# Performance work log

Hardware: AMD Instinct MI355X
Metric: run time of the kernel (lower is better)

Reference implementation:

```python
import jax, jax.numpy as jnp
import numpy as np

NE = 200000   # num_entities
NR = 16       # num_relations
D  = 128      # embed_dim
B  = 4096     # batch
S  = 64       # neighbors per node
L  = 2        # num_layers
H  = 4        # attention heads (hardcoded in module)


def _ln(x, g, b, eps=1e-5):
    m = jnp.mean(x, -1, keepdims=True)
    v = jnp.mean((x - m) ** 2, -1, keepdims=True)
    return (x - m) * jax.lax.rsqrt(v + eps) * g + b


def setup_inputs() -> dict:
    key = jax.random.key(0)
    ks = jax.random.split(key, 12)
    s = 0.05
    return {
        'drug_entity_indices': jax.random.randint(ks[0], (B,), 0, NE),
        'adj_entity': jax.random.randint(ks[1], (B, S), 0, NE),
        'adj_relation': jax.random.randint(ks[2], (B, S), 0, NR),
        'edge_weights': jax.random.uniform(ks[3], (B, S), dtype=jnp.float32),
        'entity_emb': jax.random.normal(ks[4], (NE, D), jnp.float32) * s,
        'W_rgcn': jax.random.normal(ks[5], (L, NR, D, D), jnp.float32) * s,
        'res_w': jax.random.normal(ks[6], (L, D, D), jnp.float32) * s,
        'res_b': jnp.zeros((L, D), jnp.float32),
        'proj_w': jax.random.normal(ks[7], (L, D, D), jnp.float32) * s,
        'proj_b': jnp.zeros((L, D), jnp.float32),
        'ln_g': jnp.ones((L, D), jnp.float32),
        'ln_b': jnp.zeros((L, D), jnp.float32),
        'in_proj_w': jax.random.normal(ks[8], (3 * D, D), jnp.float32) * s,
        'in_proj_b': jnp.zeros((3 * D,), jnp.float32),
        'out_proj_w': jax.random.normal(ks[9], (D, D), jnp.float32) * s,
        'out_proj_b': jnp.zeros((D,), jnp.float32),
        'fln_g': jnp.ones((D,), jnp.float32),
        'fln_b': jnp.zeros((D,), jnp.float32),
    }


def reference(drug_entity_indices, adj_entity, adj_relation, edge_weights,
              entity_emb, W_rgcn, res_w, res_b, proj_w, proj_b, ln_g, ln_b,
              in_proj_w, in_proj_b, out_proj_w, out_proj_b, fln_g, fln_b):
    node = entity_emb[drug_entity_indices]           # [B,D] combined_emb
    nbr = entity_emb[adj_entity]                     # [B,S,D]
    # Route each edge to its relation: sum_s nbr*ew*[rel==r] then one GEMM per relation
    # (mathematically identical to the per-relation masked matmul loop in torch).
    onehot = jax.nn.one_hot(adj_relation, NR, dtype=node.dtype)      # [B,S,R]
    pre = jnp.einsum('bsd,bsr->brd', nbr * edge_weights[..., None], onehot)
    outs = []
    for l in range(L):
        msgs = jnp.einsum('brd,rde->be', pre, W_rgcn[l])             # [B,D]
        h = jax.nn.relu(node + msgs + node @ res_w[l].T + res_b[l])  # RGCNAggregator
        node = _ln(h @ proj_w[l].T + proj_b[l] + node, ln_g[l], ln_b[l])
        outs.append(node)
    x = jnp.stack(outs, 0)                           # [L,B,D] seq-first
    qkv = x @ in_proj_w.T + in_proj_b
    q, k, v = jnp.split(qkv, 3, axis=-1)
    hd = D // H
    def heads(t):
        return t.reshape(L, B, H, hd).transpose(1, 2, 0, 3)          # [B,H,L,hd]
    q, k, v = heads(q), heads(k), heads(v)
    att = jax.nn.softmax(jnp.einsum('bhld,bhmd->bhlm', q, k) / np.sqrt(hd).astype(np.float32), axis=-1)
    o = jnp.einsum('bhlm,bhmd->bhld', att, v).transpose(2, 0, 1, 3).reshape(L, B, D)
    o = o @ out_proj_w.T + out_proj_b
    return _ln(o.mean(0), fln_g, fln_b)              # [B,D]
```

## Files before the change

### kernel.cpp

```cpp
#include <hip/hip_runtime.h>
#include <math.h>

#define NRREL 16
#define DDIM 128
#define BBATCH 4096
#define SNBR 64

typedef __attribute__((ext_vector_type(8))) short short8;
typedef __attribute__((ext_vector_type(4))) float floatx4;

__device__ __forceinline__ unsigned short f2bf(float f) {
    unsigned u = __builtin_bit_cast(unsigned, f);
    u += 0x7fffu + ((u >> 16) & 1u);
    return (unsigned short)(u >> 16);
}
__device__ __forceinline__ float bf2f(unsigned short u) {
    return __builtin_bit_cast(float, ((unsigned)u) << 16);
}

extern "C" __global__ __launch_bounds__(256)
void k_wconv(const float* __restrict__ W_rgcn, const float* __restrict__ res_w,
             const float* __restrict__ proj_w, const float* __restrict__ in_w,
             const float* __restrict__ out_w,
             unsigned short* __restrict__ Wcat, unsigned short* __restrict__ resw,
             unsigned short* __restrict__ projw, unsigned short* __restrict__ inw,
             unsigned short* __restrict__ outw)
{
    const int bid = blockIdx.x, t = threadIdx.x;
    if (bid < 64) {
        __shared__ float tileT[128 * 65];
        const int l = bid >> 5, k0 = (bid & 31) * 64;
        #pragma unroll
        for (int i = 0; i < 8; ++i) {
            int flat = t + 256 * i;
            int k = flat >> 5, c = flat & 31;
            float4 v = *(const float4*)(W_rgcn + ((size_t)(l * 2048 + k0 + k)) * 128 + 4 * c);
            tileT[(4 * c + 0) * 65 + k] = v.x;
            tileT[(4 * c + 1) * 65 + k] = v.y;
            tileT[(4 * c + 2) * 65 + k] = v.z;
            tileT[(4 * c + 3) * 65 + k] = v.w;
        }
        __syncthreads();
        const int e = t >> 1, half = t & 1;
        #pragma unroll
        for (int m = 0; m < 4; ++m) {
            int kk = 32 * half + 8 * m;
            short8 o;
            #pragma unroll
            for (int j = 0; j < 8; ++j) o[j] = (short)f2bf(tileT[e * 65 + kk + j]);
            *(short8*)(Wcat + ((size_t)(l * 128 + e)) * 2048 + k0 + kk) = o;
        }
    } else {
        int j4 = (bid - 64) * 1024 + t * 4;
        const float* src; unsigned short* dst; int off;
        if (j4 < 32768)       { src = res_w;  dst = resw;  off = j4; }
        else if (j4 < 65536)  { src = proj_w; dst = projw; off = j4 - 32768; }
        else if (j4 < 114688) { src = in_w;   dst = inw;   off = j4 - 65536; }
        else                  { src = out_w;  dst = outw;  off = j4 - 114688; }
        float4 v = *(const float4*)(src + off);
        ushort4 o = { f2bf(v.x), f2bf(v.y), f2bf(v.z), f2bf(v.w) };
        *(ushort4*)(dst + off) = o;
    }
}

extern "C" __global__ __launch_bounds__(256)
void k_gather(const int* __restrict__ drug, const int* __restrict__ adj_e,
              const int* __restrict__ adj_r, const float* __restrict__ ew,
              const float* __restrict__ emb,
              unsigned short* __restrict__ pre_bf, float* __restrict__ node_f)
{
    __shared__ float rows[64 * 132];
    __shared__ int   srel[64];
    __shared__ float swt[64];
    __shared__ int   sent[64];
    const int b = blockIdx.x, t = threadIdx.x;
    if (t < 64) {
        sent[t] = adj_e[b * SNBR + t];
        srel[t] = adj_r[b * SNBR + t];
        swt[t]  = ew[b * SNBR + t];
    }
    __syncthreads();
    #pragma unroll
    for (int i = 0; i < 8; ++i) {
        int flat = t + 256 * i;
        int s = flat >> 5, c = flat & 31;
        float w = swt[s];
        float4 v = *(const float4*)(emb + (size_t)sent[s] * DDIM + 4 * c);
        float4 sv; sv.x = v.x * w; sv.y = v.y * w; sv.z = v.z * w; sv.w = v.w * w;
        *(float4*)(rows + s * 132 + 4 * c) = sv;
    }
    if (t < 32) {
        float4 nf = *(const float4*)(emb + (size_t)drug[b] * DDIM + 4 * t);
        *(float4*)(node_f + (size_t)b * DDIM + 4 * t) = nf;
    }
    __syncthreads();
    const int r = t >> 4, g = t & 15;
    float acc[8] = {0.f, 0.f, 0.f, 0.f, 0.f, 0.f, 0.f, 0.f};
    #pragma unroll 4
    for (int s = 0; s < SNBR; ++s) {
        if (srel[s] == r) {
            const float* p = rows + s * 132 + 8 * g;
            #pragma unroll
            for (int j = 0; j < 8; ++j) acc[j] += p[j];
        }
    }
    short8 o;
    #pragma unroll
    for (int j = 0; j < 8; ++j) o[j] = (short)f2bf(acc[j]);
    *(short8*)(pre_bf + (size_t)b * 2048 + r * DDIM + 8 * g) = o;
}

extern "C" __global__ __launch_bounds__(256)
void k_msgs(const unsigned short* __restrict__ pre_bf,
            const unsigned short* __restrict__ Wcat, float* __restrict__ part)
{
    const int wave = threadIdx.x >> 6, wm = wave >> 1, wn = wave & 1;
    const int r0 = blockIdx.x * 64 + wm * 32;
    const int c0 = blockIdx.y * 64 + wn * 32;
    const int koff = blockIdx.z * 512;
    const int lane = threadIdx.x & 63, l15 = lane & 15, q = lane >> 4;
    floatx4 acc[2][2] = {};
    const unsigned short* a0 = pre_bf + (size_t)(r0 + l15) * 2048 + koff + q * 8;
    const unsigned short* a1 = a0 + (size_t)16 * 2048;
    const unsigned short* b0 = Wcat + (size_t)(c0 + l15) * 2048 + koff + q * 8;
    const unsigned short* b1 = b0 + (size_t)16 * 2048;
    #pragma unroll 2
    for (int k = 0; k < 512; k += 32) {
        short8 A0 = *(const short8*)(a0 + k);
        short8 A1 = *(const short8*)(a1 + k);
        short8 B0 = *(const short8*)(b0 + k);
        short8 B1 = *(const short8*)(b1 + k);
        acc[0][0] = __builtin_amdgcn_mfma_f32_16x16x32_bf16(A0, B0, acc[0][0], 0, 0, 0);
        acc[0][1] = __builtin_amdgcn_mfma_f32_16x16x32_bf16(A0, B1, acc[0][1], 0, 0, 0);
        acc[1][0] = __builtin_amdgcn_mfma_f32_16x16x32_bf16(A1, B0, acc[1][0], 0, 0, 0);
        acc[1][1] = __builtin_amdgcn_mfma_f32_16x16x32_bf16(A1, B1, acc[1][1], 0, 0, 0);
    }
    float* dst = part + (size_t)blockIdx.z * BBATCH * 256;
    for (int mi = 0; mi < 2; ++mi)
        for (int ni = 0; ni < 2; ++ni) {
            int gc = c0 + ni * 16 + l15;
            #pragma unroll
            for (int r = 0; r < 4; ++r) {
                int gr = r0 + mi * 16 + 4 * q + r;
                dst[(size_t)gr * 256 + gc] = acc[mi][ni][r];
            }
        }
}

extern "C" __global__ __launch_bounds__(256)
void k_tail(const float* __restrict__ node_fg, const float* __restrict__ part,
            const unsigned short* __restrict__ resw, const unsigned short* __restrict__ projw,
            const float* __restrict__ res_b, const float* __restrict__ proj_b,
            const float* __restrict__ ln_g, const float* __restrict__ ln_b,
            const unsigned short* __restrict__ inw, const float* __restrict__ in_b,
            const unsigned short* __restrict__ outw, const float* __restrict__ out_b,
            const float* __restrict__ fg, const float* __restrict__ fb,
            float* __restrict__ outp)
{
    __shared__ float          node_ln[32 * 132];
    __shared__ unsigned short node_b16[32 * 136];
    __shared__ unsigned short h_b16[32 * 136];
    __shared__ float          msum[32 * 260];
    __shared__ unsigned short xs_l[64 * 136];
    __shared__ unsigned short qkvl[64 * 392];
    __shared__ float          psum[2][32], psq[2][32];

    const int t = threadIdx.x, w = t >> 6, lane = t & 63, l15 = lane & 15, q = lane >> 4;
    const int r0 = blockIdx.x * 32;
    const int wm = w & 1, wn = w >> 1;

    #pragma unroll
    for (int i = 0; i < 4; ++i) {
        int flat = t + 256 * i;
        int rr = flat >> 5, c = flat & 31;
        float4 v = *(const float4*)(node_fg + (size_t)(r0 + rr) * DDIM + 4 * c);
        *(float4*)(node_ln + rr * 132 + 4 * c) = v;
        ushort4 o = { f2bf(v.x), f2bf(v.y), f2bf(v.z), f2bf(v.w) };
        *(ushort4*)(node_b16 + rr * 136 + 4 * c) = o;
    }
    #pragma unroll
    for (int i = 0; i < 8; ++i) {
        int flat = t + 256 * i;
        int rr = flat >> 6, c = flat & 63;
        float4 s = {0.f, 0.f, 0.f, 0.f};
        #pragma unroll
        for (int kc = 0; kc < 4; ++kc) {
            float4 v = *(const float4*)(part + ((size_t)kc * BBATCH + r0 + rr) * 256 + 4 * c);
            s.x += v.x; s.y += v.y; s.z += v.z; s.w += v.w;
        }
        *(float4*)(msum + rr * 260 + 4 * c) = s;
    }
    __syncthreads();

    for (int l = 0; l < 2; ++l) {
        {
            const unsigned short* Bw = resw + (size_t)l * DDIM * DDIM;
            floatx4 acc[4] = {};
            const unsigned short* ap = node_b16 + (16 * wm + l15) * 136 + 8 * q;
            #pragma unroll
            for (int kk = 0; kk < DDIM; kk += 32) {
                short8 A = *(const short8*)(ap + kk);
                #pragma unroll
                for (int ni = 0; ni < 4; ++ni) {
                    short8 B = *(const short8*)(Bw + (size_t)(64 * wn + ni * 16 + l15) * DDIM + kk + 8 * q);
                    acc[ni] = __builtin_amdgcn_mfma_f32_16x16x32_bf16(A, B, acc[ni], 0, 0, 0);
                }
            }
            #pragma unroll
            for (int ni = 0; ni < 4; ++ni) {
                int gc = 64 * wn + ni * 16 + l15;
                float rb = res_b[l * DDIM + gc];
                #pragma unroll
                for (int r = 0; r < 4; ++r) {
                    int lr = 16 * wm + 4 * q + r;
                    float v = acc[ni][r] + rb + node_ln[lr * 132 + gc] + msum[lr * 260 + l * DDIM + gc];
                    h_b16[lr * 136 + gc] = f2bf(v > 0.f ? v : 0.f);
                }
            }
        }
        __syncthreads();
        {
            const unsigned short* Bw = projw + (size_t)l * DDIM * DDIM;
            floatx4 acc[4] = {};
            const unsigned short* ap = h_b16 + (16 * wm + l15) * 136 + 8 * q;
            #pragma unroll
            for (int kk = 0; kk < DDIM; kk += 32) {
                short8 A = *(const short8*)(ap + kk);
                #pragma unroll
                for (int ni = 0; ni < 4; ++ni) {
                    short8 B = *(const short8*)(Bw + (size_t)(64 * wn + ni * 16 + l15) * DDIM + kk + 8 * q);
                    acc[ni] = __builtin_amdgcn_mfma_f32_16x16x32_bf16(A, B, acc[ni], 0, 0, 0);
                }
            }
            float vv[4][4];
            float s4[4] = {0, 0, 0, 0}, sq4[4] = {0, 0, 0, 0};
            #pragma unroll
            for (int ni = 0; ni < 4; ++ni) {
                int gc = 64 * wn + ni * 16 + l15;
                float pb = proj_b[l * DDIM + gc];
                #pragma unroll
                for (int r = 0; r < 4; ++r) {
                    int lr = 16 * wm + 4 * q + r;
                    float v = acc[ni][r] + pb + node_ln[lr * 132 + gc];
                    vv[ni][r] = v; s4[r] += v; sq4[r] += v * v;
                }
            }
            #pragma unroll
            for (int r = 0; r < 4; ++r)
                #pragma unroll
                for (int off = 8; off >= 1; off >>= 1) {
                    s4[r] += __shfl_xor(s4[r], off, 64);
                    sq4[r] += __shfl_xor(sq4[r], off, 64);
                }
            if (l15 == 0) {
                #pragma unroll
                for (int r = 0; r < 4; ++r) {
                    psum[wn][16 * wm + 4 * q + r] = s4[r];
                    psq[wn][16 * wm + 4 * q + r] = sq4[r];
                }
            }
            __syncthreads();
            #pragma unroll
            for (int ni = 0; ni < 4; ++ni) {
                int gc = 64 * wn + ni * 16 + l15;
                float g = ln_g[l * DDIM + gc], bb = ln_b[l * DDIM + gc];
                #pragma unroll
                for (int r = 0; r < 4; ++r) {
                    int lr = 16 * wm + 4 * q + r;
                    float mean = (psum[0][lr] + psum[1][lr]) * (1.f / DDIM);
                    float var = (psq[0][lr] + psq[1][lr]) * (1.f / DDIM) - mean * mean;
                    float val = (vv[ni][r] - mean) * rsqrtf(var + 1e-5f) * g + bb;
                    node_ln[lr * 132 + gc] = val;
                    unsigned short ub = f2bf(val);
                    node_b16[lr * 136 + gc] = ub;
                    xs_l[(2 * lr + l) * 136 + gc] = ub;
                }
            }
            __syncthreads();
        }
    }

    {
        floatx4 acc[24] = {};
        const unsigned short* ap = xs_l + (16 * w + l15) * 136 + 8 * q;
        #pragma unroll
        for (int kk = 0; kk < DDIM; kk += 32) {
            short8 A = *(const short8*)(ap + kk);
            #pragma unroll
            for (int ni = 0; ni < 24; ++ni) {
                short8 B = *(const short8*)(inw + (size_t)(ni * 16 + l15) * DDIM + kk + 8 * q);
                acc[ni] = __builtin_amdgcn_mfma_f32_16x16x32_bf16(A, B, acc[ni], 0, 0, 0);
            }
        }
        #pragma unroll
        for (int ni = 0; ni < 24; ++ni) {
            int gc = ni * 16 + l15;
            float ib = in_b[gc];
            #pragma unroll
            for (int r = 0; r < 4; ++r)
                qkvl[(16 * w + 4 * q + r) * 392 + gc] = f2bf(acc[ni][r] + ib);
        }
    }
    __syncthreads();

    {
        int g = t >> 3, j = t & 7;
        const unsigned short* row0 = qkvl + (2 * g) * 392;
        const unsigned short* row1 = qkvl + (2 * g + 1) * 392;
        float p00 = 0.f, p01 = 0.f, p10 = 0.f, p11 = 0.f;
        #pragma unroll
        for (int dd = 0; dd < 16; ++dd) {
            int d = 16 * j + dd;
            float q0 = bf2f(row0[d]), k0 = bf2f(row0[128 + d]);
            float q1 = bf2f(row1[d]), k1 = bf2f(row1[128 + d]);
            p00 = fmaf(q0, k0, p00); p01 = fmaf(q0, k1, p01);
            p10 = fmaf(q1, k0, p10); p11 = fmaf(q1, k1, p11);
        }
        p00 += __shfl_xor(p00, 1, 64); p01 += __shfl_xor(p01, 1, 64);
        p10 += __shfl_xor(p10, 1, 64); p11 += __shfl_xor(p11, 1, 64);
        const float sc = 0.17677669529663687f;
        p00 *= sc; p01 *= sc; p10 *= sc; p11 *= sc;
        float m0 = fmaxf(p00, p01), e00 = expf(p00 - m0), e01 = expf(p01 - m0);
        float i0 = 1.f / (e00 + e01);
        float m1 = fmaxf(p10, p11), e10 = expf(p10 - m1), e11 = expf(p11 - m1);
        float i1 = 1.f / (e10 + e11);
        #pragma unroll
        for (int dd = 0; dd < 16; ++dd) {
            int d = 16 * j + dd;
            float v0 = bf2f(row0[256 + d]), v1 = bf2f(row1[256 + d]);
            xs_l[(2 * g) * 136 + d]     = f2bf((e00 * v0 + e01 * v1) * i0);
            xs_l[(2 * g + 1) * 136 + d] = f2bf((e10 * v0 + e11 * v1) * i1);
        }
    }
    __syncthreads();

    {
        floatx4 acc[8] = {};
        const unsigned short* ap = xs_l + (16 * w + l15) * 136 + 8 * q;
        #pragma unroll
        for (int kk = 0; kk < DDIM; kk += 32) {
            short8 A = *(const short8*)(ap + kk);
            #pragma unroll
            for (int ni = 0; ni < 8; ++ni) {
                short8 B = *(const short8*)(outw + (size_t)(ni * 16 + l15) * DDIM + kk + 8 * q);
                acc[ni] = __builtin_amdgcn_mfma_f32_16x16x32_bf16(A, B, acc[ni], 0, 0, 0);
            }
        }
        float av[2][8];
        float s[2] = {0, 0}, sq[2] = {0, 0};
        #pragma unroll
        for (int ni = 0; ni < 8; ++ni) {
            int gc = ni * 16 + l15;
            float ob = out_b[gc];
            #pragma unroll
            for (int rr = 0; rr < 2; ++rr) {
                float v = 0.5f * (acc[ni][2 * rr] + acc[ni][2 * rr + 1]) + ob;
                av[rr][ni] = v; s[rr] += v; sq[rr] += v * v;
            }
        }
        #pragma unroll
        for (int rr = 0; rr < 2; ++rr)
            #pragma unroll
            for (int off = 8; off >= 1; off >>= 1) {
                s[rr] += __shfl_xor(s[rr], off, 64);
                sq[rr] += __shfl_xor(sq[rr], off, 64);
            }
        #pragma unroll
        for (int ni = 0; ni < 8; ++ni) {
            int gc = ni * 16 + l15;
            float g = fg[gc], bb = fb[gc];
            #pragma unroll
            for (int rr = 0; rr < 2; ++rr) {
                int bg = r0 + 8 * w + 2 * q + rr;
                float mean = s[rr] * (1.f / DDIM);
                float var = sq[rr] * (1.f / DDIM) - mean * mean;
                outp[(size_t)bg * DDIM + gc] = (av[rr][ni] - mean) * rsqrtf(var + 1e-5f) * g + bb;
            }
        }
    }
}

extern "C" void kernel_launch(void* const* d_in, const int* in_sizes, int n_in,
                              void* d_out, int out_size, void* d_ws, size_t ws_size,
                              hipStream_t stream) {
    const int*   drug_idx = (const int*)d_in[0];
    const int*   adj_ent  = (const int*)d_in[1];
    const int*   adj_rel  = (const int*)d_in[2];
    const float* ew       = (const float*)d_in[3];
    const float* emb      = (const float*)d_in[4];
    const float* W_rgcn   = (const float*)d_in[5];
    const float* res_w    = (const float*)d_in[6];
    const float* res_b    = (const float*)d_in[7];
    const float* proj_w   = (const float*)d_in[8];
    const float* proj_b   = (const float*)d_in[9];
    const float* ln_g     = (const float*)d_in[10];
    const float* ln_b     = (const float*)d_in[11];
    const float* in_w     = (const float*)d_in[12];
    const float* in_b     = (const float*)d_in[13];
    const float* out_w    = (const float*)d_in[14];
    const float* out_b    = (const float*)d_in[15];
    const float* fg       = (const float*)d_in[16];
    const float* fb       = (const float*)d_in[17];
    float* outp = (float*)d_out;

    char* ws = (char*)d_ws;
    size_t off = 0;
    auto alloc = [&](size_t bytes) { size_t o = off; off = (off + bytes + 255) & ~(size_t)255; return o; };
    unsigned short* pre_bf  = (unsigned short*)(ws + alloc((size_t)BBATCH * 2048 * 2));
    float*          node_f  = (float*)         (ws + alloc((size_t)BBATCH * 128 * 4));
    float*          part    = (float*)         (ws + alloc((size_t)4 * BBATCH * 256 * 4));
    unsigned short* Wcat    = (unsigned short*)(ws + alloc((size_t)256 * 2048 * 2));
    unsigned short* resw    = (unsigned short*)(ws + alloc((size_t)2 * 128 * 128 * 2));
    unsigned short* projw   = (unsigned short*)(ws + alloc((size_t)2 * 128 * 128 * 2));
    unsigned short* inw     = (unsigned short*)(ws + alloc((size_t)384 * 128 * 2));
    unsigned short* outw    = (unsigned short*)(ws + alloc((size_t)128 * 128 * 2));

    hipLaunchKernelGGL(k_wconv, dim3(192), dim3(256), 0, stream,
                       W_rgcn, res_w, proj_w, in_w, out_w, Wcat, resw, projw, inw, outw);
    hipLaunchKernelGGL(k_gather, dim3(BBATCH), dim3(256), 0, stream,
                       drug_idx, adj_ent, adj_rel, ew, emb, pre_bf, node_f);
    hipLaunchKernelGGL(k_msgs, dim3(64, 4, 4), dim3(256), 0, stream, pre_bf, Wcat, part);
    hipLaunchKernelGGL(k_tail, dim3(128), dim3(256), 0, stream,
                       node_f, part, resw, projw, res_b, proj_b, ln_g, ln_b,
                       inw, in_b, outw, out_b, fg, fb, outp);
}
```

Measured before the change: 267.3 us.

## Fuse all stages into one cooperative kernel with grid-wide syncs

Merges the weight conversion, gather, message GEMM and tail kernels into a single persistent cooperative kernel of 1024 blocks, separating the stages with grid syncs. If the cooperative launch fails it falls back to three ordinary launches. The tail now handles 8 rows per block instead of 32, which spreads it over more blocks but reloads the weights more often. The aim is to remove the launch gaps between kernels and the tail's low parallelism, at the cost of grid-barrier overhead and an occupancy cap of 4 blocks per CU with shared memory held in a union.

```diff
diff --git a/kernel.cpp b/kernel.cpp
--- a/kernel.cpp
+++ b/kernel.cpp
@@ -1,5 +1,8 @@
 #include <hip/hip_runtime.h>
+#include <hip/hip_cooperative_groups.h>
 #include <math.h>
+
+namespace cg = cooperative_groups;
 
 #define NRREL 16
 #define DDIM 128
@@ -18,363 +21,369 @@
     return __builtin_bit_cast(float, ((unsigned)u) << 16);
 }
 
-extern "C" __global__ __launch_bounds__(256)
-void k_wconv(const float* __restrict__ W_rgcn, const float* __restrict__ res_w,
-             const float* __restrict__ proj_w, const float* __restrict__ in_w,
-             const float* __restrict__ out_w,
-             unsigned short* __restrict__ Wcat, unsigned short* __restrict__ resw,
-             unsigned short* __restrict__ projw, unsigned short* __restrict__ inw,
-             unsigned short* __restrict__ outw)
-{
-    const int bid = blockIdx.x, t = threadIdx.x;
-    if (bid < 64) {
-        __shared__ float tileT[128 * 65];
-        const int l = bid >> 5, k0 = (bid & 31) * 64;
-        #pragma unroll
-        for (int i = 0; i < 8; ++i) {
-            int flat = t + 256 * i;
-            int k = flat >> 5, c = flat & 31;
-            float4 v = *(const float4*)(W_rgcn + ((size_t)(l * 2048 + k0 + k)) * 128 + 4 * c);
-            tileT[(4 * c + 0) * 65 + k] = v.x;
-            tileT[(4 * c + 1) * 65 + k] = v.y;
-            tileT[(4 * c + 2) * 65 + k] = v.z;
-            tileT[(4 * c + 3) * 65 + k] = v.w;
-        }
-        __syncthreads();
-        const int e = t >> 1, half = t & 1;
-        #pragma unroll
-        for (int m = 0; m < 4; ++m) {
-            int kk = 32 * half + 8 * m;
-            short8 o;
-            #pragma unroll
-            for (int j = 0; j < 8; ++j) o[j] = (short)f2bf(tileT[e * 65 + kk + j]);
-            *(short8*)(Wcat + ((size_t)(l * 128 + e)) * 2048 + k0 + kk) = o;
-        }
-    } else {
-        int j4 = (bid - 64) * 1024 + t * 4;
-        const float* src; unsigned short* dst; int off;
-        if (j4 < 32768)       { src = res_w;  dst = resw;  off = j4; }
-        else if (j4 < 65536)  { src = proj_w; dst = projw; off = j4 - 32768; }
-        else if (j4 < 114688) { src = in_w;   dst = inw;   off = j4 - 65536; }
-        else                  { src = out_w;  dst = outw;  off = j4 - 114688; }
-        float4 v = *(const float4*)(src + off);
-        ushort4 o = { f2bf(v.x), f2bf(v.y), f2bf(v.z), f2bf(v.w) };
-        *(ushort4*)(dst + off) = o;
-    }
-}
-
-extern "C" __global__ __launch_bounds__(256)
-void k_gather(const int* __restrict__ drug, const int* __restrict__ adj_e,
-              const int* __restrict__ adj_r, const float* __restrict__ ew,
-              const float* __restrict__ emb,
-              unsigned short* __restrict__ pre_bf, float* __restrict__ node_f)
-{
-    __shared__ float rows[64 * 132];
-    __shared__ int   srel[64];
-    __shared__ float swt[64];
-    __shared__ int   sent[64];
-    const int b = blockIdx.x, t = threadIdx.x;
-    if (t < 64) {
-        sent[t] = adj_e[b * SNBR + t];
-        srel[t] = adj_r[b * SNBR + t];
-        swt[t]  = ew[b * SNBR + t];
-    }
-    __syncthreads();
-    #pragma unroll
-    for (int i = 0; i < 8; ++i) {
-        int flat = t + 256 * i;
-        int s = flat >> 5, c = flat & 31;
-        float w = swt[s];
-        float4 v = *(const float4*)(emb + (size_t)sent[s] * DDIM + 4 * c);
-        float4 sv; sv.x = v.x * w; sv.y = v.y * w; sv.z = v.z * w; sv.w = v.w * w;
-        *(float4*)(rows + s * 132 + 4 * c) = sv;
-    }
-    if (t < 32) {
-        float4 nf = *(const float4*)(emb + (size_t)drug[b] * DDIM + 4 * t);
-        *(float4*)(node_f + (size_t)b * DDIM + 4 * t) = nf;
-    }
-    __syncthreads();
-    const int r = t >> 4, g = t & 15;
-    float acc[8] = {0.f, 0.f, 0.f, 0.f, 0.f, 0.f, 0.f, 0.f};
-    #pragma unroll 4
-    for (int s = 0; s < SNBR; ++s) {
-        if (srel[s] == r) {
-            const float* p = rows + s * 132 + 8 * g;
-            #pragma unroll
-            for (int j = 0; j < 8; ++j) acc[j] += p[j];
-        }
-    }
-    short8 o;
-    #pragma unroll
-    for (int j = 0; j < 8; ++j) o[j] = (short)f2bf(acc[j]);
-    *(short8*)(pre_bf + (size_t)b * 2048 + r * DDIM + 8 * g) = o;
-}
-
-extern "C" __global__ __launch_bounds__(256)
-void k_msgs(const unsigned short* __restrict__ pre_bf,
-            const unsigned short* __restrict__ Wcat, float* __restrict__ part)
-{
-    const int wave = threadIdx.x >> 6, wm = wave >> 1, wn = wave & 1;
-    const int r0 = blockIdx.x * 64 + wm * 32;
-    const int c0 = blockIdx.y * 64 + wn * 32;
-    const int koff = blockIdx.z * 512;
-    const int lane = threadIdx.x & 63, l15 = lane & 15, q = lane >> 4;
-    floatx4 acc[2][2] = {};
-    const unsigned short* a0 = pre_bf + (size_t)(r0 + l15) * 2048 + koff + q * 8;
-    const unsigned short* a1 = a0 + (size_t)16 * 2048;
-    const unsigned short* b0 = Wcat + (size_t)(c0 + l15) * 2048 + koff + q * 8;
-    const unsigned short* b1 = b0 + (size_t)16 * 2048;
-    #pragma unroll 2
-    for (int k = 0; k < 512; k += 32) {
-        short8 A0 = *(const short8*)(a0 + k);
-        short8 A1 = *(const short8*)(a1 + k);
-        short8 B0 = *(const short8*)(b0 + k);
-        short8 B1 = *(const short8*)(b1 + k);
-        acc[0][0] = __builtin_amdgcn_mfma_f32_16x16x32_bf16(A0, B0, acc[0][0], 0, 0, 0);
-        acc[0][1] = __builtin_amdgcn_mfma_f32_16x16x32_bf16(A0, B1, acc[0][1], 0, 0, 0);
-        acc[1][0] = __builtin_amdgcn_mfma_f32_16x16x32_bf16(A1, B0, acc[1][0], 0, 0, 0);
-        acc[1][1] = __builtin_amdgcn_mfma_f32_16x16x32_bf16(A1, B1, acc[1][1], 0, 0, 0);
-    }
-    float* dst = part + (size_t)blockIdx.z * BBATCH * 256;
-    for (int mi = 0; mi < 2; ++mi)
-        for (int ni = 0; ni < 2; ++ni) {
-            int gc = c0 + ni * 16 + l15;
-            #pragma unroll
-            for (int r = 0; r < 4; ++r) {
-                int gr = r0 + mi * 16 + 4 * q + r;
-                dst[(size_t)gr * 256 + gc] = acc[mi][ni][r];
-            }
-        }
-}
-
-extern "C" __global__ __launch_bounds__(256)
-void k_tail(const float* __restrict__ node_fg, const float* __restrict__ part,
-            const unsigned short* __restrict__ resw, const unsigned short* __restrict__ projw,
+extern "C" __global__ __launch_bounds__(256, 4)
+void k_mega(int mode,
+            const int* __restrict__ drug, const int* __restrict__ adj_e,
+            const int* __restrict__ adj_r, const float* __restrict__ ew,
+            const float* __restrict__ emb, const float* __restrict__ W_rgcn,
             const float* __restrict__ res_b, const float* __restrict__ proj_b,
             const float* __restrict__ ln_g, const float* __restrict__ ln_b,
-            const unsigned short* __restrict__ inw, const float* __restrict__ in_b,
-            const unsigned short* __restrict__ outw, const float* __restrict__ out_b,
+            const float* __restrict__ in_b, const float* __restrict__ out_b,
             const float* __restrict__ fg, const float* __restrict__ fb,
+            const float* __restrict__ res_w, const float* __restrict__ proj_w,
+            const float* __restrict__ in_w, const float* __restrict__ out_w,
+            unsigned short* __restrict__ pre_bf, float* __restrict__ node_f,
+            float* __restrict__ part, unsigned short* __restrict__ Wcat,
+            unsigned short* __restrict__ resw, unsigned short* __restrict__ projw,
+            unsigned short* __restrict__ inw, unsigned short* __restrict__ outw,
             float* __restrict__ outp)
 {
-    __shared__ float          node_ln[32 * 132];
-    __shared__ unsigned short node_b16[32 * 136];
-    __shared__ unsigned short h_b16[32 * 136];
-    __shared__ float          msum[32 * 260];
-    __shared__ unsigned short xs_l[64 * 136];
-    __shared__ unsigned short qkvl[64 * 392];
-    __shared__ float          psum[2][32], psq[2][32];
-
-    const int t = threadIdx.x, w = t >> 6, lane = t & 63, l15 = lane & 15, q = lane >> 4;
-    const int r0 = blockIdx.x * 32;
-    const int wm = w & 1, wn = w >> 1;
-
-    #pragma unroll
-    for (int i = 0; i < 4; ++i) {
-        int flat = t + 256 * i;
-        int rr = flat >> 5, c = flat & 31;
-        float4 v = *(const float4*)(node_fg + (size_t)(r0 + rr) * DDIM + 4 * c);
-        *(float4*)(node_ln + rr * 132 + 4 * c) = v;
-        ushort4 o = { f2bf(v.x), f2bf(v.y), f2bf(v.z), f2bf(v.w) };
-        *(ushort4*)(node_b16 + rr * 136 + 4 * c) = o;
+    __shared__ union {
+        struct { float rows[64 * 132]; int sent[64]; int srel[64]; float swt[64]; } g;
+        struct { float tileT[128 * 65]; } w;
+        struct {
+            float node_ln[8 * 132]; float msum[8 * 260];
+            float psum[4][8]; float psq[4][8];
+            unsigned short node_b16[8 * 136]; unsigned short h_b16[8 * 136];
+            unsigned short xs_l[16 * 136]; unsigned short qkvl[16 * 392];
+        } t;
+    } sm;
+
+    const int t = threadIdx.x, bid = blockIdx.x;
+    const int lane = t & 63, wv = t >> 6, l15 = lane & 15, q = lane >> 4;
+
+    if (mode == 0 || mode == 1) {
+        for (int rb = 0; rb < 4; ++rb) {
+            const int b = bid * 4 + rb;
+            if (t < 64) {
+                sm.g.sent[t] = adj_e[b * SNBR + t];
+                sm.g.srel[t] = adj_r[b * SNBR + t];
+                sm.g.swt[t]  = ew[b * SNBR + t];
+            }
+            __syncthreads();
+            #pragma unroll
+            for (int i = 0; i < 8; ++i) {
+                int flat = t + 256 * i;
+                int s = flat >> 5, c = flat & 31;
+                float wgt = sm.g.swt[s];
+                float4 v = *(const float4*)(emb + (size_t)sm.g.sent[s] * DDIM + 4 * c);
+                float4 sv = { v.x * wgt, v.y * wgt, v.z * wgt, v.w * wgt };
+                *(float4*)(sm.g.rows + s * 132 + 4 * c) = sv;
+            }
+            if (t < 32) {
+                float4 nf = *(const float4*)(emb + (size_t)drug[b] * DDIM + 4 * t);
+                *(float4*)(node_f + (size_t)b * DDIM + 4 * t) = nf;
+            }
+            __syncthreads();
+            const int r = t >> 4, g8 = t & 15;
+            float acc[8] = {0.f, 0.f, 0.f, 0.f, 0.f, 0.f, 0.f, 0.f};
+            for (int s = 0; s < SNBR; ++s) {
+                if (sm.g.srel[s] == r) {
+                    const float* p = sm.g.rows + s * 132 + 8 * g8;
+                    #pragma unroll
+                    for (int j = 0; j < 8; ++j) acc[j] += p[j];
+                }
+            }
+            short8 o;
+            #pragma unroll
+            for (int j = 0; j < 8; ++j) o[j] = (short)f2bf(acc[j]);
+            *(short8*)(pre_bf + (size_t)b * 2048 + r * DDIM + 8 * g8) = o;
+            __syncthreads();
+        }
+        if (bid < 64) {
+            const int l = bid >> 5, k0 = (bid & 31) * 64;
+            #pragma unroll
+            for (int i = 0; i < 8; ++i) {
+                int flat = t + 256 * i;
+                int k = flat >> 5, c = flat & 31;
+                float4 v = *(const float4*)(W_rgcn + ((size_t)(l * 2048 + k0 + k)) * 128 + 4 * c);
+                sm.w.tileT[(4 * c + 0) * 65 + k] = v.x;
+                sm.w.tileT[(4 * c + 1) * 65 + k] = v.y;
+                sm.w.tileT[(4 * c + 2) * 65 + k] = v.z;
+                sm.w.tileT[(4 * c + 3) * 65 + k] = v.w;
+            }
+            __syncthreads();
+            const int e = t >> 1, half = t & 1;
+            #pragma unroll
+            for (int m = 0; m < 4; ++m) {
+                int kk = 32 * half + 8 * m;
+                short8 o;
+                #pragma unroll
+                for (int j = 0; j < 8; ++j) o[j] = (short)f2bf(sm.w.tileT[e * 65 + kk + j]);
+                *(short8*)(Wcat + ((size_t)(l * 128 + e)) * 2048 + k0 + kk) = o;
+            }
+        } else if (bid < 192) {
+            int j4 = ((bid - 64) * 256 + t) * 4;
+            const float* src; unsigned short* dst; int off;
+            if (j4 < 32768)       { src = res_w;  dst = resw;  off = j4; }
+            else if (j4 < 65536)  { src = proj_w; dst = projw; off = j4 - 32768; }
+            else if (j4 < 114688) { src = in_w;   dst = inw;   off = j4 - 65536; }
+            else                  { src = out_w;  dst = outw;  off = j4 - 114688; }
+            float4 v = *(const float4*)(src + off);
+            ushort4 o = { f2bf(v.x), f2bf(v.y), f2bf(v.z), f2bf(v.w) };
+            *(ushort4*)(dst + off) = o;
+        }
     }
-    #pragma unroll
-    for (int i = 0; i < 8; ++i) {
-        int flat = t + 256 * i;
-        int rr = flat >> 6, c = flat & 63;
-        float4 s = {0.f, 0.f, 0.f, 0.f};
+    if (mode == 0) { __threadfence(); cg::this_grid().sync(); }
+
+    if (mode == 0 || mode == 2) {
+        const int kz = bid >> 8, rem = bid & 255, cy = rem >> 6, bx = rem & 63;
+        const int wm = wv >> 1, wn = wv & 1;
+        const int r0 = bx * 64 + wm * 32, c0 = cy * 64 + wn * 32;
+        const int koff = kz * 512;
+        floatx4 acc[2][2] = {};
+        const unsigned short* a0 = pre_bf + (size_t)(r0 + l15) * 2048 + koff + q * 8;
+        const unsigned short* a1 = a0 + (size_t)16 * 2048;
+        const unsigned short* b0 = Wcat + (size_t)(c0 + l15) * 2048 + koff + q * 8;
+        const unsigned short* b1 = b0 + (size_t)16 * 2048;
+        #pragma unroll 2
+        for (int k = 0; k < 512; k += 32) {
+            short8 A0 = *(const short8*)(a0 + k);
+            short8 A1 = *(const short8*)(a1 + k);
+            short8 B0 = *(const short8*)(b0 + k);
+            short8 B1 = *(const short8*)(b1 + k);
+            acc[0][0] = __builtin_amdgcn_mfma_f32_16x16x32_bf16(A0, B0, acc[0][0], 0, 0, 0);
+            acc[0][1] = __builtin_amdgcn_mfma_f32_16x16x32_bf16(A0, B1, acc[0][1], 0, 0, 0);
+            acc[1][0] = __builtin_amdgcn_mfma_f32_16x16x32_bf16(A1, B0, acc[1][0], 0, 0, 0);
+            acc[1][1] = __builtin_amdgcn_mfma_f32_16x16x32_bf16(A1, B1, acc[1][1], 0, 0, 0);
+        }
+        float* dst = part + (size_t)kz * BBATCH * 256;
+        for (int mi = 0; mi < 2; ++mi)
+            for (int ni = 0; ni < 2; ++ni) {
+                int gc = c0 + ni * 16 + l15;
+                #pragma unroll
+                for (int r = 0; r < 4; ++r)
+                    dst[(size_t)(r0 + mi * 16 + 4 * q + r) * 256 + gc] = acc[mi][ni][r];
+            }
+    }
+    if (mode == 0) { __threadfence(); cg::this_grid().sync(); }
+
+    if ((mode == 0 || mode == 3) && bid < 512) {
+        const int r0 = bid * 8;
+        const int cw0 = 32 * wv;
+        {
+            int rr = t >> 5, c = t & 31;
+            float4 v = *(const float4*)(node_f + (size_t)(r0 + rr) * DDIM + 4 * c);
+            *(float4*)(sm.t.node_ln + rr * 132 + 4 * c) = v;
+            ushort4 o = { f2bf(v.x), f2bf(v.y), f2bf(v.z), f2bf(v.w) };
+            *(ushort4*)(sm.t.node_b16 + rr * 136 + 4 * c) = o;
+        }
         #pragma unroll
-        for (int kc = 0; kc < 4; ++kc) {
-            float4 v = *(const float4*)(part + ((size_t)kc * BBATCH + r0 + rr) * 256 + 4 * c);
-            s.x += v.x; s.y += v.y; s.z += v.z; s.w += v.w;
-        }
-        *(float4*)(msum + rr * 260 + 4 * c) = s;
-    }
-    __syncthreads();
-
-    for (int l = 0; l < 2; ++l) {
+        for (int i = 0; i < 2; ++i) {
+            int flat = t + 256 * i;
+            int rr = flat >> 6, c = flat & 63;
+            float4 s = {0.f, 0.f, 0.f, 0.f};
+            #pragma unroll
+            for (int kc = 0; kc < 4; ++kc) {
+                float4 v = *(const float4*)(part + ((size_t)kc * BBATCH + r0 + rr) * 256 + 4 * c);
+                s.x += v.x; s.y += v.y; s.z += v.z; s.w += v.w;
+            }
+            *(float4*)(sm.t.msum + rr * 260 + 4 * c) = s;
+        }
+        __syncthreads();
+
+        for (int l = 0; l < 2; ++l) {
+            {
+                const unsigned short* Bw = resw + (size_t)l * DDIM * DDIM;
+                floatx4 acc[2] = {};
+                const unsigned short* ap = sm.t.node_b16 + l15 * 136 + 8 * q;
+                #pragma unroll
+                for (int kk = 0; kk < DDIM; kk += 32) {
+                    short8 A = *(const short8*)(ap + kk);
+                    #pragma unroll
+                    for (int ni = 0; ni < 2; ++ni) {
+                        short8 B = *(const short8*)(Bw + (size_t)(cw0 + ni * 16 + l15) * DDIM + kk + 8 * q);
+                        acc[ni] = __builtin_amdgcn_mfma_f32_16x16x32_bf16(A, B, acc[ni], 0, 0, 0);
+                    }
+                }
+                if (q < 2) {
+                    #pragma unroll
+                    for (int ni = 0; ni < 2; ++ni) {
+                        int gc = cw0 + ni * 16 + l15;
+                        float rb2 = res_b[l * DDIM + gc];
+                        #pragma unroll
+                        for (int r = 0; r < 4; ++r) {
+                            int lr = 4 * q + r;
+                            float v = acc[ni][r] + rb2 + sm.t.node_ln[lr * 132 + gc]
+                                    + sm.t.msum[lr * 260 + l * DDIM + gc];
+                            sm.t.h_b16[lr * 136 + gc] = f2bf(v > 0.f ? v : 0.f);
+                        }
+                    }
+                }
+            }
+            __syncthreads();
+            {
+                const unsigned short* Bw = projw + (size_t)l * DDIM * DDIM;
+                floatx4 acc[2] = {};
+                const unsigned short* ap = sm.t.h_b16 + l15 * 136 + 8 * q;
+                #pragma unroll
+                for (int kk = 0; kk < DDIM; kk += 32) {
+                    short8 A = *(const short8*)(ap + kk);
+                    #pragma unroll
+                    for (int ni = 0; ni < 2; ++ni) {
+                        short8 B = *(const short8*)(Bw + (size_t)(cw0 + ni * 16 + l15) * DDIM + kk + 8 * q);
+                        acc[ni] = __builtin_amdgcn_mfma_f32_16x16x32_bf16(A, B, acc[ni], 0, 0, 0);
+                    }
+                }
+                float vv[2][4];
+                float s4[4] = {0, 0, 0, 0}, sq4[4] = {0, 0, 0, 0};
+                #pragma unroll
+                for (int ni = 0; ni < 2; ++ni) {
+                    int gc = cw0 + ni * 16 + l15;
+                    float pb = proj_b[l * DDIM + gc];
+                    #pragma unroll
+                    for (int r = 0; r < 4; ++r) {
+                        int lr = 4 * q + r;
+                        float nl = (q < 2) ? sm.t.node_ln[lr * 132 + gc] : 0.f;
+                        float v = acc[ni][r] + pb + nl;
+                        vv[ni][r] = v; s4[r] += v; sq4[r] += v * v;
+                    }
+                }
+                #pragma unroll
+                for (int r = 0; r < 4; ++r)
+                    #pragma unroll
+                    for (int off2 = 8; off2 >= 1; off2 >>= 1) {
+                        s4[r] += __shfl_xor(s4[r], off2, 64);
+                        sq4[r] += __shfl_xor(sq4[r], off2, 64);
+                    }
+                if (l15 == 0 && q < 2) {
+                    #pragma unroll
+                    for (int r = 0; r < 4; ++r) {
+                        sm.t.psum[wv][4 * q + r] = s4[r];
+                        sm.t.psq[wv][4 * q + r] = sq4[r];
+                    }
+                }
+                __syncthreads();
+                if (q < 2) {
+                    #pragma unroll
+                    for (int ni = 0; ni < 2; ++ni) {
+                        int gc = cw0 + ni * 16 + l15;
+                        float g2 = ln_g[l * DDIM + gc], bb = ln_b[l * DDIM + gc];
+                        #pragma unroll
+                        for (int r = 0; r < 4; ++r) {
+                            int lr = 4 * q + r;
+                            float ssum = sm.t.psum[0][lr] + sm.t.psum[1][lr] + sm.t.psum[2][lr] + sm.t.psum[3][lr];
+                            float ssq  = sm.t.psq[0][lr] + sm.t.psq[1][lr] + sm.t.psq[2][lr] + sm.t.psq[3][lr];
+                            float mean = ssum * (1.f / DDIM);
+                            float var = ssq * (1.f / DDIM) - mean * mean;
+                            float val = (vv[ni][r] - mean) * rsqrtf(var + 1e-5f) * g2 + bb;
+                            sm.t.node_ln[lr * 132 + gc] = val;
+                            unsigned short ub = f2bf(val);
+                            sm.t.node_b16[lr * 136 + gc] = ub;
+                            sm.t.xs_l[(2 * lr + l) * 136 + gc] = ub;
+                        }
+                    }
+                }
+            }
+            __syncthreads();
+        }
+
         {
-            const unsigned short* Bw = resw + (size_t)l * DDIM * DDIM;
-            floatx4 acc[4] = {};
-            const unsigned short* ap = node_b16 + (16 * wm + l15) * 136 + 8 * q;
+            floatx4 acc[6] = {};
+            const unsigned short* ap = sm.t.xs_l + l15 * 136 + 8 * q;
             #pragma unroll
             for (int kk = 0; kk < DDIM; kk += 32) {
                 short8 A = *(const short8*)(ap + kk);
                 #pragma unroll
-                for (int ni = 0; ni < 4; ++ni) {
-                    short8 B = *(const short8*)(Bw + (size_t)(64 * wn + ni * 16 + l15) * DDIM + kk + 8 * q);
+                for (int ni = 0; ni < 6; ++ni) {
+                    short8 B = *(const short8*)(inw + (size_t)(96 * wv + ni * 16 + l15) * DDIM + kk + 8 * q);
                     acc[ni] = __builtin_amdgcn_mfma_f32_16x16x32_bf16(A, B, acc[ni], 0, 0, 0);
                 }
             }
             #pragma unroll
-            for (int ni = 0; ni < 4; ++ni) {
-                int gc = 64 * wn + ni * 16 + l15;
-                float rb = res_b[l * DDIM + gc];
-                #pragma unroll
-                for (int r = 0; r < 4; ++r) {
-                    int lr = 16 * wm + 4 * q + r;
-                    float v = acc[ni][r] + rb + node_ln[lr * 132 + gc] + msum[lr * 260 + l * DDIM + gc];
-                    h_b16[lr * 136 + gc] = f2bf(v > 0.f ? v : 0.f);
-                }
+            for (int ni = 0; ni < 6; ++ni) {
+                int gc = 96 * wv + ni * 16 + l15;
+                float ib = in_b[gc];
+                #pragma unroll
+                for (int r = 0; r < 4; ++r)
+                    sm.t.qkvl[(4 * q + r) * 392 + gc] = f2bf(acc[ni][r] + ib);
             }
         }
         __syncthreads();
+
+        if (t < 64) {
+            int g4 = t >> 3, j = t & 7;
+            const unsigned short* row0 = sm.t.qkvl + (2 * g4) * 392;
+            const unsigned short* row1 = row0 + 392;
+            float p00 = 0.f, p01 = 0.f, p10 = 0.f, p11 = 0.f;
+            #pragma unroll
+            for (int dd = 0; dd < 16; ++dd) {
+                int d = 16 * j + dd;
+                float q0 = bf2f(row0[d]), k0 = bf2f(row0[128 + d]);
+                float q1 = bf2f(row1[d]), k1 = bf2f(row1[128 + d]);
+                p00 = fmaf(q0, k0, p00); p01 = fmaf(q0, k1, p01);
+                p10 = fmaf(q1, k0, p10); p11 = fmaf(q1, k1, p11);
+            }
+            p00 += __shfl_xor(p00, 1, 64); p01 += __shfl_xor(p01, 1, 64);
+            p10 += __shfl_xor(p10, 1, 64); p11 += __shfl_xor(p11, 1, 64);
+            const float sc = 0.17677669529663687f;
+            p00 *= sc; p01 *= sc; p10 *= sc; p11 *= sc;
+            float m0 = fmaxf(p00, p01), e00 = expf(p00 - m0), e01 = expf(p01 - m0);
+            float i0 = 1.f / (e00 + e01);
+            float m1 = fmaxf(p10, p11), e10 = expf(p10 - m1), e11 = expf(p11 - m1);
+            float i1 = 1.f / (e10 + e11);
+            #pragma unroll
+            for (int dd = 0; dd < 16; ++dd) {
+                int d = 16 * j + dd;
+                float v0 = bf2f(row0[256 + d]), v1 = bf2f(row1[256 + d]);
+                sm.t.xs_l[(2 * g4) * 136 + d]     = f2bf((e00 * v0 + e01 * v1) * i0);
+                sm.t.xs_l[(2 * g4 + 1) * 136 + d] = f2bf((e10 * v0 + e11 * v1) * i1);
+            }
+        }
+        __syncthreads();
+
         {
-            const unsigned short* Bw = projw + (size_t)l * DDIM * DDIM;
-            floatx4 acc[4] = {};
-            const unsigned short* ap = h_b16 + (16 * wm + l15) * 136 + 8 * q;
+            floatx4 acc[2] = {};
+            const unsigned short* ap = sm.t.xs_l + l15 * 136 + 8 * q;
             #pragma unroll
             for (int kk = 0; kk < DDIM; kk += 32) {
                 short8 A = *(const short8*)(ap + kk);
                 #pragma unroll
-                for (int ni = 0; ni < 4; ++ni) {
-                    short8 B = *(const short8*)(Bw + (size_t)(64 * wn + ni * 16 + l15) * DDIM + kk + 8 * q);
+                for (int ni = 0; ni < 2; ++ni) {
+                    short8 B = *(const short8*)(outw + (size_t)(cw0 + ni * 16 + l15) * DDIM + kk + 8 * q);
                     acc[ni] = __builtin_amdgcn_mfma_f32_16x16x32_bf16(A, B, acc[ni], 0, 0, 0);
                 }
             }
-            float vv[4][4];
-            float s4[4] = {0, 0, 0, 0}, sq4[4] = {0, 0, 0, 0};
-            #pragma unroll
-            for (int ni = 0; ni < 4; ++ni) {
-                int gc = 64 * wn + ni * 16 + l15;
-                float pb = proj_b[l * DDIM + gc];
-                #pragma unroll
-                for (int r = 0; r < 4; ++r) {
-                    int lr = 16 * wm + 4 * q + r;
-                    float v = acc[ni][r] + pb + node_ln[lr * 132 + gc];
-                    vv[ni][r] = v; s4[r] += v; sq4[r] += v * v;
-                }
-            }
-            #pragma unroll
-            for (int r = 0; r < 4; ++r)
-                #pragma unroll
-                for (int off = 8; off >= 1; off >>= 1) {
-                    s4[r] += __shfl_xor(s4[r], off, 64);
-                    sq4[r] += __shfl_xor(sq4[r], off, 64);
+            float av[2][2];
+            float s2[2] = {0, 0}, sq2[2] = {0, 0};
+            #pragma unroll
+            for (int ni = 0; ni < 2; ++ni) {
+                int gc = cw0 + ni * 16 + l15;
+                float ob = out_b[gc];
+                #pragma unroll
+                for (int rr = 0; rr < 2; ++rr) {
+                    float v = 0.5f * (acc[ni][2 * rr] + acc[ni][2 * rr + 1]) + ob;
+                    av[ni][rr] = v; s2[rr] += v; sq2[rr] += v * v;
+                }
+            }
+            #pragma unroll
+            for (int rr = 0; rr < 2; ++rr)
+                #pragma unroll
+                for (int off2 = 8; off2 >= 1; off2 >>= 1) {
+                    s2[rr] += __shfl_xor(s2[rr], off2, 64);
+                    sq2[rr] += __shfl_xor(sq2[rr], off2, 64);
                 }
             if (l15 == 0) {
                 #pragma unroll
-                for (int r = 0; r < 4; ++r) {
-                    psum[wn][16 * wm + 4 * q + r] = s4[r];
-                    psq[wn][16 * wm + 4 * q + r] = sq4[r];
-                }
-            }
-            __syncthreads();
-            #pragma unroll
-            for (int ni = 0; ni < 4; ++ni) {
-                int gc = 64 * wn + ni * 16 + l15;
-                float g = ln_g[l * DDIM + gc], bb = ln_b[l * DDIM + gc];
-                #pragma unroll
-                for (int r = 0; r < 4; ++r) {
-                    int lr = 16 * wm + 4 * q + r;
-                    float mean = (psum[0][lr] + psum[1][lr]) * (1.f / DDIM);
-                    float var = (psq[0][lr] + psq[1][lr]) * (1.f / DDIM) - mean * mean;
-                    float val = (vv[ni][r] - mean) * rsqrtf(var + 1e-5f) * g + bb;
-                    node_ln[lr * 132 + gc] = val;
-                    unsigned short ub = f2bf(val);
-                    node_b16[lr * 136 + gc] = ub;
-                    xs_l[(2 * lr + l) * 136 + gc] = ub;
-                }
-            }
-            __syncthreads();
-        }
-    }
-
-    {
-        floatx4 acc[24] = {};
-        const unsigned short* ap = xs_l + (16 * w + l15) * 136 + 8 * q;
-        #pragma unroll
-        for (int kk = 0; kk < DDIM; kk += 32) {
-            short8 A = *(const short8*)(ap + kk);
-            #pragma unroll
-            for (int ni = 0; ni < 24; ++ni) {
-                short8 B = *(const short8*)(inw + (size_t)(ni * 16 + l15) * DDIM + kk + 8 * q);
-                acc[ni] = __builtin_amdgcn_mfma_f32_16x16x32_bf16(A, B, acc[ni], 0, 0, 0);
-            }
-        }
-        #pragma unroll
-        for (int ni = 0; ni < 24; ++ni) {
-            int gc = ni * 16 + l15;
-            float ib = in_b[gc];
-            #pragma unroll
-            for (int r = 0; r < 4; ++r)
-                qkvl[(16 * w + 4 * q + r) * 392 + gc] = f2bf(acc[ni][r] + ib);
-        }
-    }
-    __syncthreads();
-
-    {
-        int g = t >> 3, j = t & 7;
-        const unsigned short* row0 = qkvl + (2 * g) * 392;
-        const unsigned short* row1 = qkvl + (2 * g + 1) * 392;
-        float p00 = 0.f, p01 = 0.f, p10 = 0.f, p11 = 0.f;
-        #pragma unroll
-        for (int dd = 0; dd < 16; ++dd) {
-            int d = 16 * j + dd;
-            float q0 = bf2f(row0[d]), k0 = bf2f(row0[128 + d]);
-            float q1 = bf2f(row1[d]), k1 = bf2f(row1[128 + d]);
-            p00 = fmaf(q0, k0, p00); p01 = fmaf(q0, k1, p01);
-            p10 = fmaf(q1, k0, p10); p11 = fmaf(q1, k1, p11);
-        }
-        p00 += __shfl_xor(p00, 1, 64); p01 += __shfl_xor(p01, 1, 64);
-        p10 += __shfl_xor(p10, 1, 64); p11 += __shfl_xor(p11, 1, 64);
-        const float sc = 0.17677669529663687f;
-        p00 *= sc; p01 *= sc; p10 *= sc; p11 *= sc;
-        float m0 = fmaxf(p00, p01), e00 = expf(p00 - m0), e01 = expf(p01 - m0);
-        float i0 = 1.f / (e00 + e01);
-        float m1 = fmaxf(p10, p11), e10 = expf(p10 - m1), e11 = expf(p11 - m1);
-        float i1 = 1.f / (e10 + e11);
-        #pragma unroll
-        for (int dd = 0; dd < 16; ++dd) {
-            int d = 16 * j + dd;
-            float v0 = bf2f(row0[256 + d]), v1 = bf2f(row1[256 + d]);
-            xs_l[(2 * g) * 136 + d]     = f2bf((e00 * v0 + e01 * v1) * i0);
-            xs_l[(2 * g + 1) * 136 + d] = f2bf((e10 * v0 + e11 * v1) * i1);
-        }
-    }
-    __syncthreads();
-
-    {
-        floatx4 acc[8] = {};
-        const unsigned short* ap = xs_l + (16 * w + l15) * 136 + 8 * q;
-        #pragma unroll
-        for (int kk = 0; kk < DDIM; kk += 32) {
-            short8 A = *(const short8*)(ap + kk);
-            #pragma unroll
-            for (int ni = 0; ni < 8; ++ni) {
-                short8 B = *(const short8*)(outw + (size_t)(ni * 16 + l15) * DDIM + kk + 8 * q);
-                acc[ni] = __builtin_amdgcn_mfma_f32_16x16x32_bf16(A, B, acc[ni], 0, 0, 0);
-            }
-        }
-        float av[2][8];
-        float s[2] = {0, 0}, sq[2] = {0, 0};
-        #pragma unroll
-        for (int ni = 0; ni < 8; ++ni) {
-            int gc = ni * 16 + l15;
-            float ob = out_b[gc];
-            #pragma unroll
-            for (int rr = 0; rr < 2; ++rr) {
-                float v = 0.5f * (acc[ni][2 * rr] + acc[ni][2 * rr + 1]) + ob;
-                av[rr][ni] = v; s[rr] += v; sq[rr] += v * v;
-            }
-        }
-        #pragma unroll
-        for (int rr = 0; rr < 2; ++rr)
-            #pragma unroll
-            for (int off = 8; off >= 1; off >>= 1) {
-                s[rr] += __shfl_xor(s[rr], off, 64);
-                sq[rr] += __shfl_xor(sq[rr], off, 64);
-            }
-        #pragma unroll
-        for (int ni = 0; ni < 8; ++ni) {
-            int gc = ni * 16 + l15;
-            float g = fg[gc], bb = fb[gc];
-            #pragma unroll
-            for (int rr = 0; rr < 2; ++rr) {
-                int bg = r0 + 8 * w + 2 * q + rr;
-                float mean = s[rr] * (1.f / DDIM);
-                float var = sq[rr] * (1.f / DDIM) - mean * mean;
-                outp[(size_t)bg * DDIM + gc] = (av[rr][ni] - mean) * rsqrtf(var + 1e-5f) * g + bb;
+                for (int rr = 0; rr < 2; ++rr) {
+                    sm.t.psum[wv][2 * q + rr] = s2[rr];
+                    sm.t.psq[wv][2 * q + rr] = sq2[rr];
+                }
+            }
+            __syncthreads();
+            #pragma unroll
+            for (int ni = 0; ni < 2; ++ni) {
+                int gc = cw0 + ni * 16 + l15;
+                float g2 = fg[gc], bb = fb[gc];
+                #pragma unroll
+                for (int rr = 0; rr < 2; ++rr) {
+                    int bgl = 2 * q + rr;
+                    float ssum = sm.t.psum[0][bgl] + sm.t.psum[1][bgl] + sm.t.psum[2][bgl] + sm.t.psum[3][bgl];
+                    float ssq  = sm.t.psq[0][bgl] + sm.t.psq[1][bgl] + sm.t.psq[2][bgl] + sm.t.psq[3][bgl];
+                    float mean = ssum * (1.f / DDIM);
+                    float var = ssq * (1.f / DDIM) - mean * mean;
+                    outp[(size_t)(r0 + bgl) * DDIM + gc] = (av[ni][rr] - mean) * rsqrtf(var + 1e-5f) * g2 + bb;
+                }
             }
         }
     }
@@ -415,12 +424,23 @@
     unsigned short* inw     = (unsigned short*)(ws + alloc((size_t)384 * 128 * 2));
     unsigned short* outw    = (unsigned short*)(ws + alloc((size_t)128 * 128 * 2));
 
-    hipLaunchKernelGGL(k_wconv, dim3(192), dim3(256), 0, stream,
-                       W_rgcn, res_w, proj_w, in_w, out_w, Wcat, resw, projw, inw, outw);
-    hipLaunchKernelGGL(k_gather, dim3(BBATCH), dim3(256), 0, stream,
-                       drug_idx, adj_ent, adj_rel, ew, emb, pre_bf, node_f);
-    hipLaunchKernelGGL(k_msgs, dim3(64, 4, 4), dim3(256), 0, stream, pre_bf, Wcat, part);
-    hipLaunchKernelGGL(k_tail, dim3(128), dim3(256), 0, stream,
-                       node_f, part, resw, projw, res_b, proj_b, ln_g, ln_b,
-                       inw, in_b, outw, out_b, fg, fb, outp);
+    int mode = 0;
+    void* args[] = {
+        &mode, &drug_idx, &adj_ent, &adj_rel, &ew, &emb, &W_rgcn,
+        &res_b, &proj_b, &ln_g, &ln_b, &in_b, &out_b, &fg, &fb,
+        &res_w, &proj_w, &in_w, &out_w,
+        &pre_bf, &node_f, &part, &Wcat, &resw, &projw, &inw, &outw, &outp
+    };
+    hipError_t err = hipLaunchCooperativeKernel((const void*)k_mega, dim3(1024), dim3(256),
+                                                args, 0, stream);
+    if (err != hipSuccess) {
+        (void)hipGetLastError();
+        for (int m = 1; m <= 3; ++m) {
+            hipLaunchKernelGGL(k_mega, dim3(1024), dim3(256), 0, stream, m,
+                               drug_idx, adj_ent, adj_rel, ew, emb, W_rgcn,
+                               res_b, proj_b, ln_g, ln_b, in_b, out_b, fg, fb,
+                               res_w, proj_w, in_w, out_w,
+                               pre_bf, node_f, part, Wcat, resw, projw, inw, outw, outp);
+        }
+    }
 }
```

New measurement: 737.9 us. 176% more time.
